# Optimization experiments

Measured on AMD Instinct MI355X. Metric: run time of the kernel, lower is better.

The kernel has to match this reference:

```python
import jax, jax.numpy as jnp
import numpy as np

N_EMBD = 768
NUM_HEADS = 12
NEG_INF = -1e38


def setup_inputs() -> dict:
    key = jax.random.key(0)
    kx, kq, kk, kv, ko, kb = jax.random.split(key, 6)
    B, S, E = 2, 2048, N_EMBD
    scale = 1.0 / np.sqrt(E)
    return {
        "x": jax.random.normal(kx, (B, S, E), dtype=jnp.float32),
        "Wq": jax.random.normal(kq, (E, E), dtype=jnp.float32) * scale,
        "Wk": jax.random.normal(kk, (E, E), dtype=jnp.float32) * scale,
        "Wv": jax.random.normal(kv, (E, E), dtype=jnp.float32) * scale,
        "Wo": jax.random.normal(ko, (E, E), dtype=jnp.float32) * scale,
        "bo": jax.random.normal(kb, (E,), dtype=jnp.float32) * 0.01,
    }


def reference(x, Wq, Wk, Wv, Wo, bo):
    B, S, E = x.shape
    H = NUM_HEADS
    D = E // H

    def split_heads(t):  # [B,S,E] -> [B,H,S,D]
        return t.reshape(B, S, H, D).transpose(0, 2, 1, 3)

    # torch Linear (no bias): y = x @ W.T
    q = split_heads(jnp.einsum('bse,fe->bsf', x, Wq))
    k = split_heads(jnp.einsum('bse,fe->bsf', x, Wk))
    v = split_heads(jnp.einsum('bse,fe->bsf', x, Wv))

    # NOTE: original module does NOT scale by 1/sqrt(head_dim) — faithful.
    scores = jnp.einsum('bhqd,bhkd->bhqk', q, k)  # [B,H,S,S]
    causal_mask = (1.0 - jnp.tril(jnp.ones((S, S), dtype=x.dtype))) * NEG_INF
    probs = jax.nn.softmax(scores + causal_mask, axis=-1)
    attn = jnp.einsum('bhqk,bhkd->bhqd', probs, v)  # [B,H,S,D]

    merged = attn.transpose(0, 2, 1, 3).reshape(B, S, E)
    out = jnp.einsum('bse,fe->bsf', merged, Wo) + bo
    return (out, k, v)
```

## Files before the change

### kernel.cpp

```cpp
#include <hip/hip_runtime.h>
#include <hip/hip_bf16.h>

#define S_LEN 2048
#define EMB 768
#define NH 12
#define HD 64
#define L2E 1.44269504088896340736f

typedef __attribute__((ext_vector_type(8))) short short8;
typedef __attribute__((ext_vector_type(4))) float f32x4;

typedef __attribute__((address_space(3))) void lds_t;
typedef __attribute__((address_space(1))) const void gbl_t;

__device__ __forceinline__ void gload16(const void* g, void* l) {
  __builtin_amdgcn_global_load_lds((gbl_t*)g, (lds_t*)l, 16, 0, 0);
}

__device__ __forceinline__ short f2bf(float f) {
  union { float f; unsigned u; } v; v.f = f;
  unsigned r = v.u + 0x7FFFu + ((v.u >> 16) & 1u);
  return (short)(r >> 16);
}

__device__ __forceinline__ unsigned pkbf(float a, float b) {
  unsigned r;
  asm("v_cvt_pk_bf16_f32 %0, %1, %2" : "=v"(r) : "v"(a), "v"(b));
  return r;
}

__global__ void cvt_bf16(const float* __restrict__ src, short* __restrict__ dst, int n) {
  int i = (blockIdx.x * blockDim.x + threadIdx.x) * 4;
  if (i >= n) return;
  float4 v = *reinterpret_cast<const float4*>(src + i);
  short4 o;
  o.x = f2bf(v.x); o.y = f2bf(v.y); o.z = f2bf(v.z); o.w = f2bf(v.w);
  *reinterpret_cast<short4*>(dst + i) = o;
}

__global__ void cvt_w(const float* __restrict__ Wq, const float* __restrict__ Wk,
                      const float* __restrict__ Wv, const float* __restrict__ Wo,
                      short* __restrict__ Wb, short* __restrict__ Wob) {
  int sec = blockIdx.y;
  const float* src = sec == 0 ? Wq : sec == 1 ? Wk : sec == 2 ? Wv : Wo;
  short* dst = sec < 3 ? Wb + sec * 589824 : Wob;
  int i = (blockIdx.x * blockDim.x + threadIdx.x) * 4;
  float4 v = *reinterpret_cast<const float4*>(src + i);
  short4 o;
  o.x = f2bf(v.x); o.y = f2bf(v.y); o.z = f2bf(v.z); o.w = f2bf(v.w);
  *reinterpret_cast<short4*>(dst + i) = o;
}

template<int MODE>
__global__ __launch_bounds__(256)
void gemm_nt(const short* __restrict__ A, const short* __restrict__ B,
             float* __restrict__ outk, float* __restrict__ outv,
             short* __restrict__ qb, short* __restrict__ kb, short* __restrict__ vtb,
             float* __restrict__ outp, const float* __restrict__ bias) {
  const int K = EMB;
  const int NT = K / 64;
  __shared__ __align__(16) short As[2][128][64];
  __shared__ __align__(16) short Bs[2][128][64];
  int tid = threadIdx.x;
  int lane = tid & 63, wid = tid >> 6;
  int wm = wid >> 1, wn = wid & 1;
  int r16 = lane & 15, g4 = lane >> 4;
  int m0 = blockIdx.y * 128, n0 = blockIdx.x * 128;
  int lrow = lane >> 3, lchunk = lane & 7;
  int lcolsw = ((lchunk ^ lrow) * 8);
  f32x4 acc[4][4] = {};

#define STAGEG(BUF, K0) do {                                          \
    _Pragma("unroll")                                                 \
    for (int i = 0; i < 4; i++) {                                     \
      int r = wid * 32 + i * 8 + lrow;                                \
      gload16(A + (long)(m0 + r) * K + (K0) + lcolsw, &As[BUF][r][lchunk * 8]); \
      gload16(B + (long)(n0 + r) * K + (K0) + lcolsw, &Bs[BUF][r][lchunk * 8]); \
    } } while (0)

  STAGEG(0, 0);
  int cur = 0;
  for (int t = 0; t < NT; t++) {
    if (t + 1 < NT) {
      STAGEG(cur ^ 1, (t + 1) * 64);
      asm volatile("s_waitcnt vmcnt(8)" ::: "memory");
    } else {
      asm volatile("s_waitcnt vmcnt(0)" ::: "memory");
    }
    __builtin_amdgcn_sched_barrier(0);
    __builtin_amdgcn_s_barrier();
    __builtin_amdgcn_sched_barrier(0);
#pragma unroll
    for (int s = 0; s < 2; s++) {
      int csw = ((s * 4 + g4) ^ (r16 & 7)) * 8;
      short8 af[4], bf[4];
#pragma unroll
      for (int tt = 0; tt < 4; tt++) {
        af[tt] = *reinterpret_cast<const short8*>(&As[cur][wm * 64 + tt * 16 + r16][csw]);
        bf[tt] = *reinterpret_cast<const short8*>(&Bs[cur][wn * 64 + tt * 16 + r16][csw]);
      }
#pragma unroll
      for (int mt = 0; mt < 4; mt++)
#pragma unroll
        for (int nt = 0; nt < 4; nt++)
          acc[mt][nt] = __builtin_amdgcn_mfma_f32_16x16x32_bf16(af[mt], bf[nt], acc[mt][nt], 0, 0, 0);
    }
    __builtin_amdgcn_sched_barrier(0);
    __builtin_amdgcn_s_barrier();
    cur ^= 1;
  }
#undef STAGEG

#pragma unroll
  for (int mt = 0; mt < 4; mt++) {
    int nbase = m0 + wm * 64 + mt * 16 + g4 * 4;
#pragma unroll
    for (int nt = 0; nt < 4; nt++) {
      int f = n0 + wn * 64 + nt * 16 + r16;
#pragma unroll
      for (int r = 0; r < 4; r++) {
        float c = acc[mt][nt][r];
        int nn = nbase + r;
        if (MODE == 0) {
          int b = nn >> 11, s = nn & 2047;
          int sec = f / EMB; int fh = f - sec * EMB;
          int h = fh >> 6, d = fh & 63;
          int idx = (((b * NH) + h) * S_LEN + s) * HD + d;
          if (sec == 0) qb[idx] = f2bf(c);
          else if (sec == 1) { outk[idx] = c; kb[idx] = f2bf(c); }
          else {
            outv[idx] = c;
            int bh = b * NH + h;
            vtb[((long)(bh * 32 + (s >> 6)) * 64 + d) * 64 + (s & 63)] = f2bf(c);
          }
        } else {
          outp[(long)nn * EMB + f] = c + bias[f];
        }
      }
    }
  }
}

__global__ __launch_bounds__(256)
void flash_attn15(const short* __restrict__ qb, const short* __restrict__ kb,
                  const short* __restrict__ vtb, short* __restrict__ mb) {
  const int tid = threadIdx.x;
  const int w = tid >> 6, lane = tid & 63;
  const int r16 = lane & 15, g4 = lane >> 4;
  const int id = blockIdx.x;
  const int xcd = id & 7, u = id >> 3;
  const int bh = xcd + 8 * (u % 3);
  const int qt = 31 - u / 3;
  const int q0 = qt * 64 + w * 16;
  const int nkt = qt + 1;

  const short* qh = qb + (long)bh * S_LEN * HD;
  const short* kh = kb + (long)bh * S_LEN * HD;
  const short* vh = vtb + (long)bh * S_LEN * HD;

  __shared__ __align__(16) short KVl[2][2][64][64];
  __shared__ __align__(16) short Pa[4][16][40];
  __shared__ __align__(16) short Pb[4][16][40];
  __shared__ __align__(16) float sca_lds[4][16];
  float* Olds = (float*)&KVl[0][0][0][0];

  const int srow = tid >> 3, schunk = tid & 7;
  const short* ksrc = kh + srow * HD + ((schunk ^ (srow & 7)) * 8);
  const short* vsrc = vh + srow * 64 + ((schunk ^ (srow & 7)) * 8);
#define STAGE(BUF, KT) do {                                          \
    long _off = (long)(KT) * 4096;                                   \
    gload16(ksrc + _off,           &KVl[BUF][0][srow][schunk * 8]);      \
    gload16(ksrc + _off + 32 * HD, &KVl[BUF][0][srow + 32][schunk * 8]); \
    gload16(vsrc + _off,           &KVl[BUF][1][srow][schunk * 8]);      \
    gload16(vsrc + _off + 32 * 64, &KVl[BUF][1][srow + 32][schunk * 8]); \
  } while (0)

  short8 qf0 = *reinterpret_cast<const short8*>(qh + (q0 + r16) * HD + g4 * 8);
  short8 qf1 = *reinterpret_cast<const short8*>(qh + (q0 + r16) * HD + 32 + g4 * 8);

  float m0 = -1e30f, m20 = -1.44e30f;
  float l0 = 0.f;
  f32x4 oacc[4] = {};

  const int kc0 = (g4 ^ (r16 & 7)) * 8;

  STAGE(0, 0);

  for (int kt = 0; kt < nkt; kt++) {
    __syncthreads();
    if (kt + 1 < nkt) STAGE((kt + 1) & 1, kt + 1);

    const short* kbuf = &KVl[kt & 1][0][0][0];
    const short* vbuf = &KVl[kt & 1][1][0][0];

    short8 k00 = *reinterpret_cast<const short8*>(kbuf + (r16) * 64 + kc0);
    short8 k01 = *reinterpret_cast<const short8*>(kbuf + (r16) * 64 + (kc0 ^ 32));
    short8 k10 = *reinterpret_cast<const short8*>(kbuf + (16 + r16) * 64 + kc0);
    short8 k11 = *reinterpret_cast<const short8*>(kbuf + (16 + r16) * 64 + (kc0 ^ 32));
    short8 k20 = *reinterpret_cast<const short8*>(kbuf + (32 + r16) * 64 + kc0);
    short8 k21 = *reinterpret_cast<const short8*>(kbuf + (32 + r16) * 64 + (kc0 ^ 32));
    short8 k30 = *reinterpret_cast<const short8*>(kbuf + (48 + r16) * 64 + kc0);
    short8 k31 = *reinterpret_cast<const short8*>(kbuf + (48 + r16) * 64 + (kc0 ^ 32));

    f32x4 s0 = {0.f, 0.f, 0.f, 0.f}, s1 = {0.f, 0.f, 0.f, 0.f};
    f32x4 s2 = {0.f, 0.f, 0.f, 0.f}, s3 = {0.f, 0.f, 0.f, 0.f};
    s0 = __builtin_amdgcn_mfma_f32_16x16x32_bf16(k00, qf0, s0, 0, 0, 0);
    s0 = __builtin_amdgcn_mfma_f32_16x16x32_bf16(k01, qf1, s0, 0, 0, 0);
    s1 = __builtin_amdgcn_mfma_f32_16x16x32_bf16(k10, qf0, s1, 0, 0, 0);
    s1 = __builtin_amdgcn_mfma_f32_16x16x32_bf16(k11, qf1, s1, 0, 0, 0);
    s2 = __builtin_amdgcn_mfma_f32_16x16x32_bf16(k20, qf0, s2, 0, 0, 0);
    s2 = __builtin_amdgcn_mfma_f32_16x16x32_bf16(k21, qf1, s2, 0, 0, 0);
    s3 = __builtin_amdgcn_mfma_f32_16x16x32_bf16(k30, qf0, s3, 0, 0, 0);
    s3 = __builtin_amdgcn_mfma_f32_16x16x32_bf16(k31, qf1, s3, 0, 0, 0);

    if (kt == nkt - 1) {
      int qg = q0 + r16;
#pragma unroll
      for (int r = 0; r < 4; r++) {
        int kbase = kt * 64 + g4 * 4 + r;
        if (kbase > qg)      s0[r] = -1e30f;
        if (kbase + 16 > qg) s1[r] = -1e30f;
        if (kbase + 32 > qg) s2[r] = -1e30f;
        if (kbase + 48 > qg) s3[r] = -1e30f;
      }
    }

    float rm_local = fmaxf(
        fmaxf(fmaxf(fmaxf(s0[0], s0[1]), fmaxf(s0[2], s0[3])),
              fmaxf(fmaxf(s1[0], s1[1]), fmaxf(s1[2], s1[3]))),
        fmaxf(fmaxf(fmaxf(s2[0], s2[1]), fmaxf(s2[2], s2[3])),
              fmaxf(fmaxf(s3[0], s3[1]), fmaxf(s3[2], s3[3]))));

    if (!__all(rm_local <= m0 + 8.f)) {
      float x = rm_local;
      x = fmaxf(x, __shfl_xor(x, 16));
      x = fmaxf(x, __shfl_xor(x, 32));
      float nm = fmaxf(m0, x);
      float sca = __builtin_exp2f((m0 - nm) * L2E);
      m0 = nm; m20 = nm * L2E; l0 *= sca;
      if (g4 == 0) sca_lds[w][r16] = sca;
      f32x4 sr = *reinterpret_cast<const f32x4*>(&sca_lds[w][g4 * 4]);
#pragma unroll
      for (int dt = 0; dt < 4; dt++)
#pragma unroll
        for (int r = 0; r < 4; r++) oacc[dt][r] *= sr[r];
    }

    float rs = 0.f;
#pragma unroll
    for (int r = 0; r < 4; r++) {
      s0[r] = __builtin_exp2f(fmaf(s0[r], L2E, -m20));
      s1[r] = __builtin_exp2f(fmaf(s1[r], L2E, -m20));
      s2[r] = __builtin_exp2f(fmaf(s2[r], L2E, -m20));
      s3[r] = __builtin_exp2f(fmaf(s3[r], L2E, -m20));
      rs += (s0[r] + s1[r]) + (s2[r] + s3[r]);
    }
    l0 += rs;

    {
      uint2 wv;
      wv.x = pkbf(s0[0], s0[1]); wv.y = pkbf(s0[2], s0[3]);
      *reinterpret_cast<uint2*>(&Pa[w][r16][g4 * 4]) = wv;
      wv.x = pkbf(s1[0], s1[1]); wv.y = pkbf(s1[2], s1[3]);
      *reinterpret_cast<uint2*>(&Pa[w][r16][16 + g4 * 4]) = wv;
      wv.x = pkbf(s2[0], s2[1]); wv.y = pkbf(s2[2], s2[3]);
      *reinterpret_cast<uint2*>(&Pb[w][r16][g4 * 4]) = wv;
      wv.x = pkbf(s3[0], s3[1]); wv.y = pkbf(s3[2], s3[3]);
      *reinterpret_cast<uint2*>(&Pb[w][r16][16 + g4 * 4]) = wv;
    }
    short8 pa0 = *reinterpret_cast<const short8*>(&Pa[w][r16][g4 * 8]);
    short8 pa1 = *reinterpret_cast<const short8*>(&Pb[w][r16][g4 * 8]);

    short8 v00 = *reinterpret_cast<const short8*>(vbuf + (r16) * 64 + kc0);
    short8 v01 = *reinterpret_cast<const short8*>(vbuf + (r16) * 64 + (kc0 ^ 32));
    short8 v10 = *reinterpret_cast<const short8*>(vbuf + (16 + r16) * 64 + kc0);
    short8 v11 = *reinterpret_cast<const short8*>(vbuf + (16 + r16) * 64 + (kc0 ^ 32));
    short8 v20 = *reinterpret_cast<const short8*>(vbuf + (32 + r16) * 64 + kc0);
    short8 v21 = *reinterpret_cast<const short8*>(vbuf + (32 + r16) * 64 + (kc0 ^ 32));
    short8 v30 = *reinterpret_cast<const short8*>(vbuf + (48 + r16) * 64 + kc0);
    short8 v31 = *reinterpret_cast<const short8*>(vbuf + (48 + r16) * 64 + (kc0 ^ 32));

    oacc[0] = __builtin_amdgcn_mfma_f32_16x16x32_bf16(pa0, v00, oacc[0], 0, 0, 0);
    oacc[0] = __builtin_amdgcn_mfma_f32_16x16x32_bf16(pa1, v01, oacc[0], 0, 0, 0);
    oacc[1] = __builtin_amdgcn_mfma_f32_16x16x32_bf16(pa0, v10, oacc[1], 0, 0, 0);
    oacc[1] = __builtin_amdgcn_mfma_f32_16x16x32_bf16(pa1, v11, oacc[1], 0, 0, 0);
    oacc[2] = __builtin_amdgcn_mfma_f32_16x16x32_bf16(pa0, v20, oacc[2], 0, 0, 0);
    oacc[2] = __builtin_amdgcn_mfma_f32_16x16x32_bf16(pa1, v21, oacc[2], 0, 0, 0);
    oacc[3] = __builtin_amdgcn_mfma_f32_16x16x32_bf16(pa0, v30, oacc[3], 0, 0, 0);
    oacc[3] = __builtin_amdgcn_mfma_f32_16x16x32_bf16(pa1, v31, oacc[3], 0, 0, 0);
  }
#undef STAGE

  __syncthreads();

  {
    float rs = l0;
    rs += __shfl_xor(rs, 16);
    rs += __shfl_xor(rs, 32);
    if (g4 == 0) sca_lds[w][r16] = rs;
  }
  f32x4 li = *reinterpret_cast<const f32x4*>(&sca_lds[w][g4 * 4]);
  f32x4 iv;
#pragma unroll
  for (int r = 0; r < 4; r++) iv[r] = 1.f / li[r];
  float* Ow = Olds + w * 16 * 68;
#pragma unroll
  for (int dt = 0; dt < 4; dt++)
#pragma unroll
    for (int r = 0; r < 4; r++)
      Ow[(g4 * 4 + r) * 68 + dt * 16 + r16] = oacc[dt][r] * iv[r];
  {
    int orow = lane >> 2, oc = (lane & 3) * 16;
    int bb = bh / NH, h = bh % NH;
    f32x4 a0 = *reinterpret_cast<const f32x4*>(&Ow[orow * 68 + oc]);
    f32x4 a1 = *reinterpret_cast<const f32x4*>(&Ow[orow * 68 + oc + 4]);
    f32x4 a2 = *reinterpret_cast<const f32x4*>(&Ow[orow * 68 + oc + 8]);
    f32x4 a3 = *reinterpret_cast<const f32x4*>(&Ow[orow * 68 + oc + 12]);
    short8 sa, sb;
#pragma unroll
    for (int j = 0; j < 4; j++) {
      sa[j] = f2bf(a0[j]); sa[4 + j] = f2bf(a1[j]);
      sb[j] = f2bf(a2[j]); sb[4 + j] = f2bf(a3[j]);
    }
    short* dst = &mb[((long)(bb * S_LEN + q0 + orow)) * EMB + h * HD + oc];
    *reinterpret_cast<short8*>(dst) = sa;
    *reinterpret_cast<short8*>(dst + 8) = sb;
  }
}

extern "C" void kernel_launch(void* const* d_in, const int* in_sizes, int n_in,
                              void* d_out, int out_size, void* d_ws, size_t ws_size,
                              hipStream_t stream) {
  const float* x  = (const float*)d_in[0];
  const float* Wq = (const float*)d_in[1];
  const float* Wk = (const float*)d_in[2];
  const float* Wv = (const float*)d_in[3];
  const float* Wo = (const float*)d_in[4];
  const float* bo = (const float*)d_in[5];

  float* out  = (float*)d_out;
  float* outk = out + 3145728;
  float* outv = out + 6291456;

  short* ws  = (short*)d_ws;
  short* xb  = ws;
  short* Wb  = xb + 3145728;
  short* Wob = Wb + 1769472;
  short* qb  = Wob + 589824;
  short* kb  = qb + 3145728;
  short* vtb = kb + 3145728;
  short* mb  = vtb + 3145728;

  cvt_bf16<<<3072, 256, 0, stream>>>(x, xb, 3145728);
  cvt_w<<<dim3(576, 4), 256, 0, stream>>>(Wq, Wk, Wv, Wo, Wb, Wob);

  gemm_nt<0><<<dim3(18, 32), 256, 0, stream>>>(xb, Wb, outk, outv, qb, kb, vtb, nullptr, nullptr);
  flash_attn15<<<768, 256, 0, stream>>>(qb, kb, vtb, mb);
  gemm_nt<1><<<dim3(6, 32), 256, 0, stream>>>(mb, Wob, nullptr, nullptr, nullptr, nullptr, nullptr, out, bo);
}
```

Before: 112.4 us.

## Stage QKV GEMM epilogue through LDS for coalesced stores; merge conversion kernels

The QKV projection epilogue now writes its accumulator tile into shared memory, which reuses the GEMM staging buffers, and then emits row-contiguous vectorized stores for Q, K (fp32 and bf16) and V fp32. The transposed bf16 V is written directly from registers as short4 vectors. The x and weight fp32-to-bf16 conversions are merged into a single launch. The goal is to replace scattered scalar per-element global writes with coalesced wide stores and to cut one kernel launch, at the cost of a larger LDS footprint and an extra barrier.

```diff
diff --git a/kernel.cpp b/kernel.cpp
--- a/kernel.cpp
+++ b/kernel.cpp
@@ -29,26 +29,28 @@
   return r;
 }
 
-__global__ void cvt_bf16(const float* __restrict__ src, short* __restrict__ dst, int n) {
-  int i = (blockIdx.x * blockDim.x + threadIdx.x) * 4;
-  if (i >= n) return;
-  float4 v = *reinterpret_cast<const float4*>(src + i);
+__global__ void cvt_all(const float* __restrict__ x,
+                        const float* __restrict__ Wq, const float* __restrict__ Wk,
+                        const float* __restrict__ Wv, const float* __restrict__ Wo,
+                        short* __restrict__ xb, short* __restrict__ Wb,
+                        short* __restrict__ Wob) {
+  int bid = blockIdx.x, tid = threadIdx.x;
+  const float* src;
+  short* dst;
+  int off;
+  if (bid < 3072) {
+    src = x; dst = xb; off = bid * 1024 + tid * 4;
+  } else {
+    int wb = bid - 3072;
+    int sec = wb / 576;
+    off = (wb % 576) * 1024 + tid * 4;
+    src = sec == 0 ? Wq : sec == 1 ? Wk : sec == 2 ? Wv : Wo;
+    dst = sec < 3 ? Wb + sec * 589824 : Wob;
+  }
+  float4 v = *reinterpret_cast<const float4*>(src + off);
   short4 o;
   o.x = f2bf(v.x); o.y = f2bf(v.y); o.z = f2bf(v.z); o.w = f2bf(v.w);
-  *reinterpret_cast<short4*>(dst + i) = o;
-}
-
-__global__ void cvt_w(const float* __restrict__ Wq, const float* __restrict__ Wk,
-                      const float* __restrict__ Wv, const float* __restrict__ Wo,
-                      short* __restrict__ Wb, short* __restrict__ Wob) {
-  int sec = blockIdx.y;
-  const float* src = sec == 0 ? Wq : sec == 1 ? Wk : sec == 2 ? Wv : Wo;
-  short* dst = sec < 3 ? Wb + sec * 589824 : Wob;
-  int i = (blockIdx.x * blockDim.x + threadIdx.x) * 4;
-  float4 v = *reinterpret_cast<const float4*>(src + i);
-  short4 o;
-  o.x = f2bf(v.x); o.y = f2bf(v.y); o.z = f2bf(v.z); o.w = f2bf(v.w);
-  *reinterpret_cast<short4*>(dst + i) = o;
+  *reinterpret_cast<short4*>(dst + off) = o;
 }
 
 template<int MODE>
@@ -59,8 +61,10 @@
              float* __restrict__ outp, const float* __restrict__ bias) {
   const int K = EMB;
   const int NT = K / 64;
-  __shared__ __align__(16) short As[2][128][64];
-  __shared__ __align__(16) short Bs[2][128][64];
+  __shared__ __align__(16) char RAW[128 * 132 * 4];
+  short (*As)[128][64] = (short(*)[128][64])RAW;
+  short (*Bs)[128][64] = (short(*)[128][64])(RAW + 32768);
+  float (*Cl)[132] = (float(*)[132])RAW;
   int tid = threadIdx.x;
   int lane = tid & 63, wid = tid >> 6;
   int wm = wid >> 1, wn = wid & 1;
@@ -111,31 +115,93 @@
   }
 #undef STAGEG
 
+  if (MODE == 1) {
+#pragma unroll
+    for (int mt = 0; mt < 4; mt++) {
+      int nbase = m0 + wm * 64 + mt * 16 + g4 * 4;
+#pragma unroll
+      for (int nt = 0; nt < 4; nt++) {
+        int f = n0 + wn * 64 + nt * 16 + r16;
+#pragma unroll
+        for (int r = 0; r < 4; r++)
+          outp[(long)(nbase + r) * EMB + f] = acc[mt][nt][r] + bias[f];
+      }
+    }
+    return;
+  }
+
+  const int bx = blockIdx.x;
+  const int sec = bx / 6;
+  const int h0 = (bx % 6) * 2;
+  const int b = m0 >> 11, s0l = m0 & 2047;
+
+  if (sec == 2) {
+#pragma unroll
+    for (int mt = 0; mt < 4; mt++) {
+      int sg = s0l + wm * 64 + mt * 16 + g4 * 4;
+#pragma unroll
+      for (int nt = 0; nt < 4; nt++) {
+        int fl = wn * 64 + nt * 16 + r16;
+        int h = h0 + (fl >> 6), d = fl & 63;
+        int bh = b * NH + h;
+        short4 o;
+        o.x = f2bf(acc[mt][nt][0]); o.y = f2bf(acc[mt][nt][1]);
+        o.z = f2bf(acc[mt][nt][2]); o.w = f2bf(acc[mt][nt][3]);
+        *reinterpret_cast<short4*>(
+            &vtb[((long)(bh * 32 + (sg >> 6)) * 64 + d) * 64 + (sg & 63)]) = o;
+      }
+    }
+  }
+
 #pragma unroll
   for (int mt = 0; mt < 4; mt++) {
-    int nbase = m0 + wm * 64 + mt * 16 + g4 * 4;
+    int rl = wm * 64 + mt * 16 + g4 * 4;
 #pragma unroll
     for (int nt = 0; nt < 4; nt++) {
-      int f = n0 + wn * 64 + nt * 16 + r16;
-#pragma unroll
-      for (int r = 0; r < 4; r++) {
-        float c = acc[mt][nt][r];
-        int nn = nbase + r;
-        if (MODE == 0) {
-          int b = nn >> 11, s = nn & 2047;
-          int sec = f / EMB; int fh = f - sec * EMB;
-          int h = fh >> 6, d = fh & 63;
-          int idx = (((b * NH) + h) * S_LEN + s) * HD + d;
-          if (sec == 0) qb[idx] = f2bf(c);
-          else if (sec == 1) { outk[idx] = c; kb[idx] = f2bf(c); }
-          else {
-            outv[idx] = c;
-            int bh = b * NH + h;
-            vtb[((long)(bh * 32 + (s >> 6)) * 64 + d) * 64 + (s & 63)] = f2bf(c);
-          }
-        } else {
-          outp[(long)nn * EMB + f] = c + bias[f];
+      int fl = wn * 64 + nt * 16 + r16;
+#pragma unroll
+      for (int r = 0; r < 4; r++) Cl[rl + r][fl] = acc[mt][nt][r];
+    }
+  }
+  __syncthreads();
+
+  {
+    int row = tid >> 1, cb = (tid & 1) * 32;
+#pragma unroll
+    for (int hh = 0; hh < 2; hh++) {
+      const float* src = &Cl[row][hh * 64 + cb];
+      long base = ((long)(b * NH + h0 + hh) * S_LEN + s0l) * HD + (long)row * 64 + cb;
+      if (sec == 0) {
+        short* dq = qb + base;
+#pragma unroll
+        for (int c = 0; c < 4; c++) {
+          f32x4 a = *reinterpret_cast<const f32x4*>(src + c * 8);
+          f32x4 bb = *reinterpret_cast<const f32x4*>(src + c * 8 + 4);
+          short8 o;
+#pragma unroll
+          for (int j = 0; j < 4; j++) { o[j] = f2bf(a[j]); o[4 + j] = f2bf(bb[j]); }
+          *reinterpret_cast<short8*>(dq + c * 8) = o;
         }
+      } else if (sec == 1) {
+        float* dk = outk + base;
+        short* dkb = kb + base;
+#pragma unroll
+        for (int c = 0; c < 4; c++) {
+          f32x4 a = *reinterpret_cast<const f32x4*>(src + c * 8);
+          f32x4 bb = *reinterpret_cast<const f32x4*>(src + c * 8 + 4);
+          *reinterpret_cast<f32x4*>(dk + c * 8) = a;
+          *reinterpret_cast<f32x4*>(dk + c * 8 + 4) = bb;
+          short8 o;
+#pragma unroll
+          for (int j = 0; j < 4; j++) { o[j] = f2bf(a[j]); o[4 + j] = f2bf(bb[j]); }
+          *reinterpret_cast<short8*>(dkb + c * 8) = o;
+        }
+      } else {
+        float* dv = outv + base;
+#pragma unroll
+        for (int c = 0; c < 8; c++)
+          *reinterpret_cast<f32x4*>(dv + c * 4) =
+              *reinterpret_cast<const f32x4*>(src + c * 4);
       }
     }
   }
@@ -351,8 +417,7 @@
   short* vtb = kb + 3145728;
   short* mb  = vtb + 3145728;
 
-  cvt_bf16<<<3072, 256, 0, stream>>>(x, xb, 3145728);
-  cvt_w<<<dim3(576, 4), 256, 0, stream>>>(Wq, Wk, Wv, Wo, Wb, Wob);
+  cvt_all<<<5376, 256, 0, stream>>>(x, Wq, Wk, Wv, Wo, xb, Wb, Wob);
 
   gemm_nt<0><<<dim3(18, 32), 256, 0, stream>>>(xb, Wb, outk, outv, qb, kb, vtb, nullptr, nullptr);
   flash_attn15<<<768, 256, 0, stream>>>(qb, kb, vtb, mb);
```

After: 103.4 us. 8.0% less time.
